# Performance work log

Measured on AMD Instinct MI355X. Metric: run time of the kernel, lower is better.

Reference implementation:

```python
import jax, jax.numpy as jnp
import numpy as np

B, D, H, V = 64, 1024, 8, 32000
OFF = 0  # pad/ignore token id
W_BCE, W_LB, W_ENT, W_BUDGET = 1.0, 0.2, 0.01, 0.05


def setup_inputs() -> dict:
    key = jax.random.key(0)
    ks = jax.random.split(key, 6)
    hidden = jax.random.normal(ks[0], (B, D), dtype=jnp.float32)
    router_w1 = jax.random.normal(ks[1], (4 * D, D), dtype=jnp.float32) * 0.02
    router_b1 = jnp.zeros((4 * D,), dtype=jnp.float32)
    router_w2 = jax.random.normal(ks[2], (H, 4 * D), dtype=jnp.float32) * 0.02
    router_b2 = jnp.zeros((H,), dtype=jnp.float32)
    heads_w = jax.random.normal(ks[3], (H, D, V), dtype=jnp.float32) * 0.02
    labels = jax.random.randint(ks[4], (B, H), 0, V, dtype=jnp.int64)
    return {
        'hidden': hidden,
        'router_w1': router_w1, 'router_b1': router_b1,
        'router_w2': router_w2, 'router_b2': router_b2,
        'heads_w': heads_w,
        'labels': labels,
        'k_max': 2,
    }


def reference(hidden, router_w1, router_b1, router_w2, router_b2, heads_w, labels, k_max):
    nH = router_b2.shape[0]
    # Router: Linear -> exact GELU -> Linear
    r = jax.nn.gelu(hidden @ router_w1.T + router_b1, approximate=False)
    gate_logits = r @ router_w2.T + router_b2              # [B, H]
    # Eval routing: top-k -> active mask (one_hot(topk).sum(2).bool())
    _, topk = jax.lax.top_k(gate_logits, k_max)            # [B, k]
    active = jnp.sum(jax.nn.one_hot(topk, nH, dtype=jnp.int32), axis=1) > 0  # [B, H]
    # All H heads applied to the same hidden state -> single fused GEMM
    logits = jnp.einsum('bd,hdv->bhv', hidden, heads_w)    # [B, H, V]
    # Masked cross-entropy with ignore_index == OFF (mean over valid entries)
    logp = jax.nn.log_softmax(logits, axis=-1)
    nll = -jnp.take_along_axis(logp, labels[:, :, None], axis=-1)[..., 0]  # [B, H]
    valid = active & (labels != OFF)
    n_valid = jnp.maximum(jnp.sum(valid), 1)
    ce = jnp.sum(jnp.where(valid, nll, 0.0)) / n_valid
    # BCE-with-logits against active mask (teacher_mask=None path)
    tgt = active.astype(jnp.float32)
    g = gate_logits
    bce = jnp.mean(jnp.maximum(g, 0.0) - g * tgt + jnp.log1p(jnp.exp(-jnp.abs(g))))
    # Load-balance
    freq = tgt.mean(axis=0)
    lb = jnp.sum((freq - 1.0 / nH) ** 2)
    # Router entropy
    p = jax.nn.softmax(g, axis=-1)
    ent = -jnp.mean(jnp.sum(p * jnp.log(p + 1e-9), axis=-1))
    budget = tgt.mean()
    loss = ce + W_BCE * bce + W_LB * lb + W_ENT * ent + W_BUDGET * budget
    return logits, gate_logits, active, loss
```

## Files before the change

kernel.cpp:

```cpp
#include <hip/hip_runtime.h>
#include <cstdint>
#include <cstddef>

#define BB 64
#define DD 1024
#define HH 8
#define VV 32000
#define H4 4096
#define NBLK 125

#define OFF_HHI    0
#define OFF_HLO    32768
#define OFF_R      65536
#define OFF_NLL    327680
#define OFF_CNT    328192
#define OFF_SCAL   328704
#define OFF_PMAX   330000
#define OFF_PSUM   394000

#define OFF_LOGITS 0
#define OFF_GATE   16384000
#define OFF_ACT    16384512
#define OFF_LOSS   16385024

typedef __attribute__((ext_vector_type(8))) _Float16 f16x8;
typedef __attribute__((ext_vector_type(4))) float f32x4;

__global__ void k_h2f16split(const float* __restrict__ in,
                             _Float16* __restrict__ hi_out,
                             _Float16* __restrict__ lo_out) {
    int i = blockIdx.x * 256 + threadIdx.x;
    float x = in[i];
    _Float16 hi = (_Float16)x;
    hi_out[i] = hi;
    lo_out[i] = (_Float16)(x - (float)hi);
}

__global__ __launch_bounds__(64) void k_router1(
    const float* __restrict__ w1, const _Float16* __restrict__ hhi,
    const _Float16* __restrict__ hlo, const float* __restrict__ b1,
    float* __restrict__ r) {
    const int j0 = blockIdx.x * 16;
    const int lane = threadIdx.x;
    const int lg = lane >> 4, lr = lane & 15;
    const float* wp = w1 + (size_t)(j0 + lr) * DD + lg * 8;

    f32x4 acc[4];
#pragma unroll
    for (int nt = 0; nt < 4; ++nt) acc[nt] = (f32x4){0.f, 0.f, 0.f, 0.f};

    for (int kc = 0; kc < DD; kc += 32) {
        float4 a0 = *(const float4*)(wp + kc);
        float4 a1 = *(const float4*)(wp + kc + 4);
        float av[8] = {a0.x, a0.y, a0.z, a0.w, a1.x, a1.y, a1.z, a1.w};
        f16x8 fahi, falo;
#pragma unroll
        for (int j = 0; j < 8; ++j) {
            _Float16 h16 = (_Float16)av[j];
            fahi[j] = h16;
            falo[j] = (_Float16)(av[j] - (float)h16);
        }
#pragma unroll
        for (int nt = 0; nt < 4; ++nt) {
            size_t boff = (size_t)(nt * 16 + lr) * DD + kc + lg * 8;
            f16x8 fbhi = *(const f16x8*)(hhi + boff);
            f16x8 fblo = *(const f16x8*)(hlo + boff);
            acc[nt] = __builtin_amdgcn_mfma_f32_16x16x32_f16(fahi, fbhi, acc[nt], 0, 0, 0);
            acc[nt] = __builtin_amdgcn_mfma_f32_16x16x32_f16(fahi, fblo, acc[nt], 0, 0, 0);
            acc[nt] = __builtin_amdgcn_mfma_f32_16x16x32_f16(falo, fbhi, acc[nt], 0, 0, 0);
        }
    }

#pragma unroll
    for (int nt = 0; nt < 4; ++nt) {
        int b = nt * 16 + lr;
        int j = j0 + lg * 4;
        float4 o;
        float* ov = (float*)&o;
#pragma unroll
        for (int q = 0; q < 4; ++q) {
            float s = acc[nt][q] + b1[j + q];
            ov[q] = 0.5f * s * (1.0f + erff(s * 0.70710678118654752f));
        }
        *(float4*)&r[(size_t)b * H4 + j] = o;
    }
}

__global__ void k_router2(const float* __restrict__ r, const float* __restrict__ w2,
                          const float* __restrict__ b2, float* __restrict__ gate) {
    int b = blockIdx.x;
    int h = threadIdx.x >> 5;
    int lane = threadIdx.x & 31;
    const float* rr = r + (size_t)b * H4;
    const float* ww = w2 + (size_t)h * H4;
    float s = 0.f;
    for (int j = lane; j < H4; j += 32) s = fmaf(rr[j], ww[j], s);
    for (int off = 16; off > 0; off >>= 1) s += __shfl_down(s, off, 32);
    if (lane == 0) gate[b * HH + h] = s + b2[h];
}

__global__ void k_routing_aux(const float* __restrict__ gate, const int* __restrict__ kmaxp,
                              float* __restrict__ act_out, float* __restrict__ scal) {
    __shared__ float af[64][8];
    __shared__ float bces[64], ents[64];
    int b = threadIdx.x;
    float g[8];
#pragma unroll
    for (int h = 0; h < 8; ++h) g[h] = gate[b * 8 + h];
    int k = kmaxp[0]; k = k < 0 ? 0 : (k > 8 ? 8 : k);
    bool act[8] = {false, false, false, false, false, false, false, false};
    for (int s = 0; s < k; ++s) {
        int best = -1; float bv = -1e30f;
#pragma unroll
        for (int h = 0; h < 8; ++h)
            if (!act[h] && g[h] > bv) { bv = g[h]; best = h; }
        act[best] = true;
    }
    float m = -1e30f;
#pragma unroll
    for (int h = 0; h < 8; ++h) m = fmaxf(m, g[h]);
    float se = 0.f, ex[8];
#pragma unroll
    for (int h = 0; h < 8; ++h) { ex[h] = expf(g[h] - m); se += ex[h]; }
    float bce = 0.f, ent = 0.f;
#pragma unroll
    for (int h = 0; h < 8; ++h) {
        float t = act[h] ? 1.f : 0.f;
        bce += fmaxf(g[h], 0.f) - g[h] * t + log1pf(expf(-fabsf(g[h])));
        float p = ex[h] / se;
        ent -= p * logf(p + 1e-9f);
        af[b][h] = t;
        act_out[b * 8 + h] = t;
    }
    bces[b] = bce; ents[b] = ent;
    __syncthreads();
    if (b == 0) {
        float bsum = 0.f, esum = 0.f, asum = 0.f, lb = 0.f;
        for (int i = 0; i < 64; ++i) { bsum += bces[i]; esum += ents[i]; }
        for (int h = 0; h < 8; ++h) {
            float f = 0.f;
            for (int i = 0; i < 64; ++i) f += af[i][h];
            asum += f;
            float fr = f / 64.f - 0.125f;
            lb += fr * fr;
        }
        scal[0] = bsum / 512.f;
        scal[1] = lb;
        scal[2] = esum / 64.f;
        scal[3] = asum / 512.f;
    }
}

#define BM 256
#define BK 32

__global__ __launch_bounds__(256) void k_heads_gemm(
    const float* __restrict__ W, const _Float16* __restrict__ hA,
    float* __restrict__ out, float* __restrict__ pmax, float* __restrict__ psum) {
    __shared__ __align__(16) float ldsA[2][BK][256];
    const int h  = blockIdx.y;
    const int blk = blockIdx.x;
    const int v0 = blk * BM;
    const int tid = threadIdx.x;
    const int wv = tid >> 6, lane = tid & 63;
    const int lg = lane >> 4, lr = lane & 15;

    const float* wbase = W + (size_t)h * DD * VV + v0;

#define STAGE(kc_, buf_)                                                        \
    {                                                                           \
        _Pragma("unroll")                                                       \
        for (int i_ = 0; i_ < 8; ++i_) {                                        \
            int r_ = wv + 4 * i_;                                               \
            const float* src_ = wbase + (size_t)((kc_) * BK + r_) * VV          \
                                + ((lane ^ (r_ >> 3)) << 2);                    \
            __builtin_amdgcn_global_load_lds(                                   \
                (const __attribute__((address_space(1))) unsigned int*)src_,    \
                (__attribute__((address_space(3))) unsigned int*)&ldsA[buf_][r_][0], \
                16, 0, 0);                                                      \
        }                                                                       \
    }

    f32x4 acc[4][4];
#pragma unroll
    for (int vt = 0; vt < 4; ++vt)
#pragma unroll
        for (int nt = 0; nt < 4; ++nt) acc[vt][nt] = (f32x4){0.f, 0.f, 0.f, 0.f};

    STAGE(0, 0);
    asm volatile("s_waitcnt vmcnt(0)" ::: "memory");
    __syncthreads();

    for (int kc = 0; kc < DD / BK; ++kc) {
        const int cur = kc & 1;

        f16x8 fb[4];
#pragma unroll
        for (int nt = 0; nt < 4; ++nt)
            fb[nt] = *(const f16x8*)(hA + (size_t)(nt * 16 + lr) * DD + kc * BK + lg * 8);

        if (kc < DD / BK - 1) STAGE(kc + 1, cur ^ 1);

        const int vq_base = wv * 16 + (lr >> 2);
#pragma unroll
        for (int vt = 0; vt < 4; ++vt) {
            const int p = (vq_base + vt * 4) ^ lg;
            const float* col = &ldsA[cur][lg * 8][(p << 2) + (lr & 3)];
            f16x8 fa;
#pragma unroll
            for (int j = 0; j < 8; ++j) fa[j] = (_Float16)col[j * 256];
#pragma unroll
            for (int nt = 0; nt < 4; ++nt)
                acc[vt][nt] = __builtin_amdgcn_mfma_f32_16x16x32_f16(fa, fb[nt], acc[vt][nt], 0, 0, 0);
        }

        asm volatile("s_waitcnt vmcnt(0)" ::: "memory");
        __syncthreads();
    }

    float* sm = &ldsA[0][0][0];
#pragma unroll
    for (int vt = 0; vt < 4; ++vt) {
#pragma unroll
        for (int nt = 0; nt < 4; ++nt) {
            int b = nt * 16 + lr;
            int vcol = wv * 64 + vt * 16 + lg * 4;
            int col = vcol ^ ((b & 7) << 2);
            *(f32x4*)&sm[b * 256 + col] = acc[vt][nt];
        }
    }
    __syncthreads();

#pragma unroll
    for (int bb = 0; bb < 16; ++bb) {
        int b = wv * 16 + bb;
        int col = (lane * 4) ^ ((b & 7) << 2);
        f32x4 vv = *(const f32x4*)&sm[b * 256 + col];
        *(float4*)&out[((size_t)b * HH + h) * VV + v0 + lane * 4] = *(float4*)&vv;
        float mx = fmaxf(fmaxf(vv[0], vv[1]), fmaxf(vv[2], vv[3]));
#pragma unroll
        for (int off = 32; off > 0; off >>= 1)
            mx = fmaxf(mx, __shfl_xor(mx, off));
        float se = expf(vv[0] - mx) + expf(vv[1] - mx) + expf(vv[2] - mx) + expf(vv[3] - mx);
#pragma unroll
        for (int off = 32; off > 0; off >>= 1)
            se += __shfl_xor(se, off);
        if (lane == 0) {
            pmax[(size_t)(b * HH + h) * NBLK + blk] = mx;
            psum[(size_t)(b * HH + h) * NBLK + blk] = se;
        }
    }
#undef STAGE
}

__global__ __launch_bounds__(64) void k_ce_finish(
    const float* __restrict__ pmax, const float* __restrict__ psum,
    const float* __restrict__ logits, const float* __restrict__ act,
    const int* __restrict__ labels, float* __restrict__ nllv, float* __restrict__ cnt) {
    int p = blockIdx.x;
    int lane = threadIdx.x;
    float m = -1e30f, s = 0.f;
    for (int i = lane; i < NBLK; i += 64) {
        float m2 = pmax[(size_t)p * NBLK + i];
        float s2 = psum[(size_t)p * NBLK + i];
        float M = fmaxf(m, m2);
        s = s * expf(m - M) + s2 * expf(m2 - M);
        m = M;
    }
#pragma unroll
    for (int off = 32; off > 0; off >>= 1) {
        float m2 = __shfl_xor(m, off);
        float s2 = __shfl_xor(s, off);
        float M = fmaxf(m, m2);
        s = s * expf(m - M) + s2 * expf(m2 - M);
        m = M;
    }
    if (lane == 0) {
        int lab = labels[p];
        float lv = logits[(size_t)p * VV + lab];
        float nll = -(lv - m - logf(s));
        bool valid = (act[p] > 0.5f) && (lab != 0);
        nllv[p] = valid ? nll : 0.f;
        cnt[p]  = valid ? 1.f : 0.f;
    }
}

__global__ void k_final_loss(const float* __restrict__ nllv, const float* __restrict__ cnt,
                             const float* __restrict__ scal, float* __restrict__ lossp) {
    __shared__ float r1[256], r2[256];
    float a = nllv[threadIdx.x] + nllv[threadIdx.x + 256];
    float c = cnt[threadIdx.x]  + cnt[threadIdx.x + 256];
    r1[threadIdx.x] = a; r2[threadIdx.x] = c; __syncthreads();
    for (int s = 128; s > 0; s >>= 1) {
        if (threadIdx.x < s) { r1[threadIdx.x] += r1[threadIdx.x + s]; r2[threadIdx.x] += r2[threadIdx.x + s]; }
        __syncthreads();
    }
    if (threadIdx.x == 0) {
        float nv = r2[0] < 1.f ? 1.f : r2[0];
        float ce = r1[0] / nv;
        lossp[0] = ce + 1.0f * scal[0] + 0.2f * scal[1] + 0.01f * scal[2] + 0.05f * scal[3];
    }
}

extern "C" void kernel_launch(void* const* d_in, const int* in_sizes, int n_in,
                              void* d_out, int out_size, void* d_ws, size_t ws_size,
                              hipStream_t stream) {
    const float* hidden = (const float*)d_in[0];
    const float* w1     = (const float*)d_in[1];
    const float* b1     = (const float*)d_in[2];
    const float* w2     = (const float*)d_in[3];
    const float* b2     = (const float*)d_in[4];
    const float* W      = (const float*)d_in[5];
    const int*   labels = (const int*)d_in[6];
    const int*   kmaxp  = (const int*)d_in[7];

    float* ws  = (float*)d_ws;
    float* out = (float*)d_out;

    _Float16* hhi = (_Float16*)(ws + OFF_HHI);
    _Float16* hlo = (_Float16*)(ws + OFF_HLO);
    float* r     = ws + OFF_R;
    float* nllv  = ws + OFF_NLL;
    float* cntv  = ws + OFF_CNT;
    float* scal  = ws + OFF_SCAL;
    float* pmax  = ws + OFF_PMAX;
    float* psum  = ws + OFF_PSUM;

    float* logits = out + OFF_LOGITS;
    float* gate   = out + OFF_GATE;
    float* activ  = out + OFF_ACT;
    float* lossp  = out + OFF_LOSS;

    k_h2f16split<<<dim3(256), 256, 0, stream>>>(hidden, hhi, hlo);
    k_router1<<<dim3(256), 64, 0, stream>>>(w1, hhi, hlo, b1, r);
    k_router2<<<dim3(64), 256, 0, stream>>>(r, w2, b2, gate);
    k_routing_aux<<<dim3(1), 64, 0, stream>>>(gate, kmaxp, activ, scal);
    k_heads_gemm<<<dim3(NBLK, 8), 256, 0, stream>>>(W, hhi, logits, pmax, psum);
    k_ce_finish<<<dim3(512), 64, 0, stream>>>(pmax, psum, logits, activ, labels, nllv, cntv);
    k_final_loss<<<dim3(1), 256, 0, stream>>>(nllv, cntv, scal, lossp);
}
```

Baseline: 343.3 us.

## Single-buffer heads GEMM LDS and raise occupancy with two-pass epilogue

The heads GEMM drops its double-buffered LDS tile for a single 32KB buffer and sets launch bounds to 4 blocks per CU, so more workgroups can hide the latency of the weight stream. The epilogue now writes the accumulator tile through LDS in two 32-row passes so it fits the smaller buffer. The grid is flattened to 1D with the head index in the low bits, so neighbouring blocks cover different heads at the same vocab offset. The cost is that prefetch overlap within a block is gone: each k-step waits on its own load, then on a barrier.

After: 358.5 us. +4.4%, slower.

```diff
diff --git a/kernel.cpp b/kernel.cpp
--- a/kernel.cpp
+++ b/kernel.cpp
@@ -7,6 +7,8 @@
 #define HH 8
 #define VV 32000
 #define H4 4096
+#define BM 256
+#define BK 32
 #define NBLK 125
 
 #define OFF_HHI    0
@@ -151,61 +153,50 @@
     }
 }
 
-#define BM 256
-#define BK 32
-
-__global__ __launch_bounds__(256) void k_heads_gemm(
+__global__ __launch_bounds__(256, 4) void k_heads_gemm(
     const float* __restrict__ W, const _Float16* __restrict__ hA,
     float* __restrict__ out, float* __restrict__ pmax, float* __restrict__ psum) {
-    __shared__ __align__(16) float ldsA[2][BK][256];
-    const int h  = blockIdx.y;
-    const int blk = blockIdx.x;
-    const int v0 = blk * BM;
+    __shared__ __align__(16) float ldsA[BK][256];
+    const int bid = blockIdx.x;
+    const int h   = bid & 7;
+    const int blk = bid >> 3;
+    const int v0  = blk * BM;
     const int tid = threadIdx.x;
     const int wv = tid >> 6, lane = tid & 63;
     const int lg = lane >> 4, lr = lane & 15;
 
     const float* wbase = W + (size_t)h * DD * VV + v0;
 
-#define STAGE(kc_, buf_)                                                        \
-    {                                                                           \
-        _Pragma("unroll")                                                       \
-        for (int i_ = 0; i_ < 8; ++i_) {                                        \
-            int r_ = wv + 4 * i_;                                               \
-            const float* src_ = wbase + (size_t)((kc_) * BK + r_) * VV          \
-                                + ((lane ^ (r_ >> 3)) << 2);                    \
-            __builtin_amdgcn_global_load_lds(                                   \
-                (const __attribute__((address_space(1))) unsigned int*)src_,    \
-                (__attribute__((address_space(3))) unsigned int*)&ldsA[buf_][r_][0], \
-                16, 0, 0);                                                      \
-        }                                                                       \
-    }
-
     f32x4 acc[4][4];
 #pragma unroll
     for (int vt = 0; vt < 4; ++vt)
 #pragma unroll
         for (int nt = 0; nt < 4; ++nt) acc[vt][nt] = (f32x4){0.f, 0.f, 0.f, 0.f};
 
-    STAGE(0, 0);
-    asm volatile("s_waitcnt vmcnt(0)" ::: "memory");
-    __syncthreads();
-
     for (int kc = 0; kc < DD / BK; ++kc) {
-        const int cur = kc & 1;
+#pragma unroll
+        for (int i_ = 0; i_ < 8; ++i_) {
+            int r_ = wv + 4 * i_;
+            const float* src_ = wbase + (size_t)(kc * BK + r_) * VV
+                                + ((lane ^ (r_ >> 3)) << 2);
+            __builtin_amdgcn_global_load_lds(
+                (const __attribute__((address_space(1))) unsigned int*)src_,
+                (__attribute__((address_space(3))) unsigned int*)&ldsA[r_][0],
+                16, 0, 0);
+        }
+        asm volatile("s_waitcnt vmcnt(0)" ::: "memory");
+        asm volatile("s_barrier" ::: "memory");
 
         f16x8 fb[4];
 #pragma unroll
         for (int nt = 0; nt < 4; ++nt)
             fb[nt] = *(const f16x8*)(hA + (size_t)(nt * 16 + lr) * DD + kc * BK + lg * 8);
 
-        if (kc < DD / BK - 1) STAGE(kc + 1, cur ^ 1);
-
         const int vq_base = wv * 16 + (lr >> 2);
 #pragma unroll
         for (int vt = 0; vt < 4; ++vt) {
             const int p = (vq_base + vt * 4) ^ lg;
-            const float* col = &ldsA[cur][lg * 8][(p << 2) + (lr & 3)];
+            const float* col = &ldsA[lg * 8][(p << 2) + (lr & 3)];
             f16x8 fa;
 #pragma unroll
             for (int j = 0; j < 8; ++j) fa[j] = (_Float16)col[j * 256];
@@ -214,43 +205,50 @@
                 acc[vt][nt] = __builtin_amdgcn_mfma_f32_16x16x32_f16(fa, fb[nt], acc[vt][nt], 0, 0, 0);
         }
 
-        asm volatile("s_waitcnt vmcnt(0)" ::: "memory");
+        asm volatile("s_waitcnt lgkmcnt(0)" ::: "memory");
+        asm volatile("s_barrier" ::: "memory");
+    }
+
+    float* sm = &ldsA[0][0];
+#pragma unroll
+    for (int pass = 0; pass < 2; ++pass) {
+#pragma unroll
+        for (int nt2 = 0; nt2 < 2; ++nt2) {
+            int nt = pass * 2 + nt2;
+            int b = nt * 16 + lr;
+            int brow = nt2 * 16 + lr;
+#pragma unroll
+            for (int vt = 0; vt < 4; ++vt) {
+                int vcol = wv * 64 + vt * 16 + lg * 4;
+                int col = vcol ^ ((b & 7) << 2);
+                *(f32x4*)&sm[brow * 256 + col] = acc[vt][nt];
+            }
+        }
         __syncthreads();
-    }
-
-    float* sm = &ldsA[0][0][0];
-#pragma unroll
-    for (int vt = 0; vt < 4; ++vt) {
-#pragma unroll
-        for (int nt = 0; nt < 4; ++nt) {
-            int b = nt * 16 + lr;
-            int vcol = wv * 64 + vt * 16 + lg * 4;
-            int col = vcol ^ ((b & 7) << 2);
-            *(f32x4*)&sm[b * 256 + col] = acc[vt][nt];
-        }
-    }
-    __syncthreads();
-
-#pragma unroll
-    for (int bb = 0; bb < 16; ++bb) {
-        int b = wv * 16 + bb;
-        int col = (lane * 4) ^ ((b & 7) << 2);
-        f32x4 vv = *(const f32x4*)&sm[b * 256 + col];
-        *(float4*)&out[((size_t)b * HH + h) * VV + v0 + lane * 4] = *(float4*)&vv;
-        float mx = fmaxf(fmaxf(vv[0], vv[1]), fmaxf(vv[2], vv[3]));
-#pragma unroll
-        for (int off = 32; off > 0; off >>= 1)
-            mx = fmaxf(mx, __shfl_xor(mx, off));
-        float se = expf(vv[0] - mx) + expf(vv[1] - mx) + expf(vv[2] - mx) + expf(vv[3] - mx);
-#pragma unroll
-        for (int off = 32; off > 0; off >>= 1)
-            se += __shfl_xor(se, off);
-        if (lane == 0) {
-            pmax[(size_t)(b * HH + h) * NBLK + blk] = mx;
-            psum[(size_t)(b * HH + h) * NBLK + blk] = se;
-        }
-    }
-#undef STAGE
+#pragma unroll
+        for (int i = 0; i < 8; ++i) {
+            int fid = tid + i * 256;
+            int brow = fid >> 6;
+            int c4 = fid & 63;
+            int b = pass * 32 + brow;
+            int col = (c4 * 4) ^ ((b & 7) << 2);
+            f32x4 vv = *(const f32x4*)&sm[brow * 256 + col];
+            *(float4*)&out[((size_t)b * HH + h) * VV + v0 + c4 * 4] = *(float4*)&vv;
+            float mx = fmaxf(fmaxf(vv[0], vv[1]), fmaxf(vv[2], vv[3]));
+#pragma unroll
+            for (int off = 32; off > 0; off >>= 1)
+                mx = fmaxf(mx, __shfl_xor(mx, off));
+            float se = expf(vv[0] - mx) + expf(vv[1] - mx) + expf(vv[2] - mx) + expf(vv[3] - mx);
+#pragma unroll
+            for (int off = 32; off > 0; off >>= 1)
+                se += __shfl_xor(se, off);
+            if (lane == 0) {
+                pmax[(size_t)(b * HH + h) * NBLK + blk] = mx;
+                psum[(size_t)(b * HH + h) * NBLK + blk] = se;
+            }
+        }
+        __syncthreads();
+    }
 }
 
 __global__ __launch_bounds__(64) void k_ce_finish(
@@ -335,7 +333,7 @@
     k_router1<<<dim3(256), 64, 0, stream>>>(w1, hhi, hlo, b1, r);
     k_router2<<<dim3(64), 256, 0, stream>>>(r, w2, b2, gate);
     k_routing_aux<<<dim3(1), 64, 0, stream>>>(gate, kmaxp, activ, scal);
-    k_heads_gemm<<<dim3(NBLK, 8), 256, 0, stream>>>(W, hhi, logits, pmax, psum);
+    k_heads_gemm<<<dim3(NBLK * 8), 256, 0, stream>>>(W, hhi, logits, pmax, psum);
     k_ce_finish<<<dim3(512), 64, 0, stream>>>(pmax, psum, logits, activ, labels, nllv, cntv);
     k_final_loss<<<dim3(1), 256, 0, stream>>>(nllv, cntv, scal, lossp);
 }
```
